# Performance work log

Measured on AMD Instinct MI355X. Metric: run time of the kernel, lower is better.

## Reference

```python
import jax, jax.numpy as jnp
import numpy as np

B, L, D, H, BS, R, MLP = 2, 4096, 768, 12, 64, 3, 3072
HD = D // H            # 64 head dim
NB = L // BS           # 64 blocks
EPS = 1e-6
SEED = 0               # connectivity_seed


def _rand_plan():
    """Static BigBird key-block plan for middle query blocks: [NB-2, 5+R].
    Columns: global first, global last, window (i-1, i, i+1), R random blocks."""
    rng = np.random.RandomState(SEED)
    rows = []
    for i in range(1, NB - 1):
        excl = {0, NB - 1, i - 1, i, i + 1}
        cand = np.array([j for j in range(NB) if j not in excl])
        rnd = rng.choice(cand, size=R, replace=False)
        rows.append(np.concatenate([np.array([0, NB - 1, i - 1, i, i + 1]), rnd]))
    return jnp.asarray(np.stack(rows), dtype=jnp.int32)

_PLAN = _rand_plan()


def _layernorm(x, scale, bias):
    mu = jnp.mean(x, axis=-1, keepdims=True)
    var = jnp.mean(jnp.square(x - mu), axis=-1, keepdims=True)
    return (x - mu) * jax.lax.rsqrt(var + EPS) * scale + bias


def _bigbird_attention(x, Wq, Wk, Wv, Wo):
    # projections: [B,L,D] x [D,H,HD] -> [B,H,L,HD]; flax scales q by 1/sqrt(HD)
    q = jnp.einsum('bld,dhk->bhlk', x, Wq) / jnp.sqrt(jnp.asarray(HD, x.dtype))
    k = jnp.einsum('bld,dhk->bhlk', x, Wk)
    v = jnp.einsum('bld,dhk->bhlk', x, Wv)
    qb = q.reshape(B, H, NB, BS, HD)
    kb = k.reshape(B, H, NB, BS, HD)
    vb = v.reshape(B, H, NB, BS, HD)
    # global query rows (first & last block) attend densely to all keys
    qg = qb[:, :, jnp.array([0, NB - 1])]                 # [B,H,2,BS,HD]
    sg = jnp.einsum('bhgqd,bhld->bhgql', qg, k)           # [B,H,2,BS,L]
    og = jnp.einsum('bhgql,bhld->bhgqd', jax.nn.softmax(sg, axis=-1), v)
    # middle query rows: gather window + global + random key blocks
    S = _PLAN.shape[1]                                     # 5 + R = 8 blocks
    km = kb[:, :, _PLAN].reshape(B, H, NB - 2, S * BS, HD)
    vm = vb[:, :, _PLAN].reshape(B, H, NB - 2, S * BS, HD)
    sm = jnp.einsum('bhmqd,bhmkd->bhmqk', qb[:, :, 1:NB - 1], km)
    om = jnp.einsum('bhmqk,bhmkd->bhmqd', jax.nn.softmax(sm, axis=-1), vm)
    ob = jnp.concatenate([og[:, :, :1], om, og[:, :, 1:]], axis=2)  # [B,H,NB,BS,HD]
    o = ob.reshape(B, H, L, HD)
    return jnp.einsum('bhlk,hkd->bld', o, Wo)


def setup_inputs() -> dict:
    key = jax.random.key(0)
    ks = jax.random.split(key, 8)
    s_qkv = (2.0 / (D + HD)) ** 0.5   # xavier-uniform-ish std
    s_mlp1 = (2.0 / (D + MLP)) ** 0.5
    return {
        'x': jax.random.normal(ks[0], (B, L, D), jnp.float32),
        'ln1_scale': jnp.ones((D,), jnp.float32),
        'ln1_bias': jnp.zeros((D,), jnp.float32),
        'Wq': jax.random.normal(ks[1], (D, H, HD), jnp.float32) * s_qkv,
        'Wk': jax.random.normal(ks[2], (D, H, HD), jnp.float32) * s_qkv,
        'Wv': jax.random.normal(ks[3], (D, H, HD), jnp.float32) * s_qkv,
        'Wo': jax.random.normal(ks[4], (H, HD, D), jnp.float32) * s_qkv,
        'ln2_scale': jnp.ones((D,), jnp.float32),
        'ln2_bias': jnp.zeros((D,), jnp.float32),
        'W1': jax.random.normal(ks[5], (D, MLP), jnp.float32) * s_mlp1,
        'b1': jnp.zeros((MLP,), jnp.float32),
        'W2': jax.random.normal(ks[6], (MLP, D), jnp.float32) * s_mlp1,
        'b2': jnp.zeros((D,), jnp.float32),
    }


def reference(x, ln1_scale, ln1_bias, Wq, Wk, Wv, Wo, ln2_scale, ln2_bias, W1, b1, W2, b2):
    h = _layernorm(x, ln1_scale, ln1_bias)
    attn = _bigbird_attention(h, Wq, Wk, Wv, Wo)
    x1 = attn + x                                  # residual (dropout deterministic)
    y = _layernorm(x1, ln2_scale, ln2_bias)
    y = jax.nn.relu(jnp.einsum('bld,df->blf', y, W1) + b1)
    y = jnp.einsum('blf,fd->bld', y, W2) + b2
    return x1 + y
```

## Files before the change

### kernel.cpp

```cpp
#include <hip/hip_runtime.h>
#include <stdint.h>

constexpr int D_MODEL = 768;
constexpr int SEQ     = 4096;
constexpr int NHEAD   = 12;
constexpr int HDIM    = 64;
constexpr int BATCH   = 2;
constexpr int DFF     = 3072;
constexpr int ROWS    = BATCH * SEQ;

typedef __attribute__((ext_vector_type(8))) __bf16 bfrag;
typedef __attribute__((ext_vector_type(8))) short  s16x8;
typedef __attribute__((ext_vector_type(4))) short  s16x4;
typedef __attribute__((ext_vector_type(4))) float  f32x4;

#define MFMA16(a, b, c) __builtin_amdgcn_mfma_f32_16x16x32_bf16((a), (b), (c), 0, 0, 0)
#define AS1(p) ((__attribute__((address_space(1))) void*)(uintptr_t)(p))
#define AS3(p) ((__attribute__((address_space(3))) void*)(p))

__device__ __forceinline__ float b2f(short s) {
  union { unsigned u; float f; } c;
  c.u = ((unsigned)(unsigned short)s) << 16;
  return c.f;
}
__device__ __forceinline__ short f2b(float f) {
  union { float f; unsigned u; } c;
  c.f = f;
  unsigned r = c.u + 0x7fffu + ((c.u >> 16) & 1u);
  return (short)(r >> 16);
}

struct PlanT { int v[64][8]; };

struct MTRng {
  unsigned mt[624];
  int mti;
  constexpr MTRng() : mt{}, mti(624) {
    mt[0] = 0u;
    for (int i = 1; i < 624; ++i)
      mt[i] = 1812433253u * (mt[i-1] ^ (mt[i-1] >> 30)) + (unsigned)i;
  }
  constexpr unsigned next() {
    if (mti >= 624) {
      for (int i = 0; i < 624; ++i) {
        unsigned y = (mt[i] & 0x80000000u) | (mt[(i+1) % 624] & 0x7fffffffu);
        unsigned v = mt[(i+397) % 624] ^ (y >> 1);
        if (y & 1u) v ^= 0x9908b0dfu;
        mt[i] = v;
      }
      mti = 0;
    }
    unsigned y = mt[mti++];
    y ^= y >> 11;
    y ^= (y << 7)  & 0x9d2c5680u;
    y ^= (y << 15) & 0xefc60000u;
    y ^= y >> 18;
    return y;
  }
  constexpr unsigned interval(unsigned mx) {
    unsigned mask = mx;
    mask |= mask >> 1; mask |= mask >> 2; mask |= mask >> 4;
    mask |= mask >> 8; mask |= mask >> 16;
    unsigned v = next() & mask;
    while (v > mx) v = next() & mask;
    return v;
  }
};

constexpr PlanT make_plan() {
  PlanT P{};
  MTRng rng{};
  for (int i = 1; i <= 62; ++i) {
    int cand[64] = {}; int n = 0;
    for (int j = 0; j < 64; ++j) {
      if (j == 0 || j == 63 || j == i-1 || j == i || j == i+1) continue;
      cand[n++] = j;
    }
    int perm[64] = {};
    for (int p = 0; p < n; ++p) perm[p] = p;
    for (int p = n - 1; p > 0; --p) {
      int j = (int)rng.interval((unsigned)p);
      int t = perm[p]; perm[p] = perm[j]; perm[j] = t;
    }
    P.v[i][0] = 0;  P.v[i][1] = 63; P.v[i][2] = i-1; P.v[i][3] = i; P.v[i][4] = i+1;
    P.v[i][5] = cand[perm[0]]; P.v[i][6] = cand[perm[1]]; P.v[i][7] = cand[perm[2]];
  }
  return P;
}
constexpr PlanT h_plan = make_plan();
__constant__ PlanT g_plan = h_plan;

__global__ __launch_bounds__(256) void ln_kernel(
    const float* __restrict__ x, const float* __restrict__ sc,
    const float* __restrict__ bi, short* __restrict__ y)
{
  const int row = blockIdx.x, tid = threadIdx.x;
  const size_t base = (size_t)row * D_MODEL;
  float v0 = x[base + tid], v1 = x[base + tid + 256], v2 = x[base + tid + 512];
  float s  = v0 + v1 + v2;
  float s2 = v0*v0 + v1*v1 + v2*v2;
  for (int off = 1; off < 64; off <<= 1) {
    s  += __shfl_xor(s,  off);
    s2 += __shfl_xor(s2, off);
  }
  __shared__ float red[8];
  if ((tid & 63) == 0) { red[tid >> 6] = s; red[4 + (tid >> 6)] = s2; }
  __syncthreads();
  s  = red[0] + red[1] + red[2] + red[3];
  s2 = red[4] + red[5] + red[6] + red[7];
  const float mu  = s * (1.f / 768.f);
  const float var = s2 * (1.f / 768.f) - mu * mu;
  const float rs  = rsqrtf(var + 1e-6f);
  short* yr = y + base;
  yr[tid]       = f2b((v0 - mu) * rs * sc[tid]       + bi[tid]);
  yr[tid + 256] = f2b((v1 - mu) * rs * sc[tid + 256] + bi[tid + 256]);
  yr[tid + 512] = f2b((v2 - mu) * rs * sc[tid + 512] + bi[tid + 512]);
}

struct TrArgs { const float* src[6]; short* dst[6]; };

__global__ __launch_bounds__(256) void tr_all(TrArgs a) {
  __shared__ short tile[32][33];
  const int idx = blockIdx.x;
  int w, bx, by, Rr, Cc;
  if (idx < 2304)      { w = idx / 576; int t = idx % 576;  bx = t % 24; by = t / 24; Rr = 768;  Cc = 768;  }
  else if (idx < 4608) { w = 4;         int t = idx - 2304; bx = t % 96; by = t / 96; Rr = 768;  Cc = 3072; }
  else                 { w = 5;         int t = idx - 4608; bx = t % 24; by = t / 24; Rr = 3072; Cc = 768;  }
  const float* in = a.src[w];
  short* out = a.dst[w];
  const int x0 = bx * 32, y0 = by * 32;
  const int tx = threadIdx.x & 31, ty = threadIdx.x >> 5;
  for (int i = 0; i < 32; i += 8)
    tile[ty + i][tx] = f2b(in[(size_t)(y0 + ty + i) * Cc + x0 + tx]);
  __syncthreads();
  for (int i = 0; i < 32; i += 8)
    out[(size_t)(x0 + ty + i) * Rr + y0 + tx] = tile[tx][ty + i];
}

enum { M_QKV = 0, M_RES = 3, M_BRELU = 4, M_BRES = 5 };

template <int MODE, int TN>
__global__ __launch_bounds__(256) void gemm_bt(
    const short* __restrict__ A, const short* __restrict__ Bt,
    void* __restrict__ Cv, short* __restrict__ C2, short* __restrict__ C3,
    const float* __restrict__ res, const float* __restrict__ bias, int N, int K)
{
  constexpr int NT = TN / 32;
  alignas(16) __shared__ short As[3][128 * 32];
  alignas(16) __shared__ short Bs[3][TN * 32];
  const int tid = threadIdx.x;
  const int wave = tid >> 6, lane = tid & 63;
  const int quad = lane >> 4, l15 = lane & 15;
  const int m0 = blockIdx.x * 128, n0 = blockIdx.y * TN;
  const int mw = (wave & 1) * 64, nw = (wave >> 1) * (TN / 2);

  f32x4 acc[4][NT];
#pragma unroll
  for (int i = 0; i < 4; ++i)
#pragma unroll
    for (int j = 0; j < NT; ++j) acc[i][j] = f32x4{0.f, 0.f, 0.f, 0.f};

  const int srow = wave * 32 + (lane >> 2);
  const int scol = (lane & 3) * 8;
  const size_t arow = (size_t)(m0 + srow) * K + scol;
  const size_t brow128 = (size_t)(n0 + srow) * K + scol;
  const size_t brow64  = (size_t)(n0 + wave * 16 + (lane >> 2)) * K + scol;

  auto STAGE = [&](int buf, int k0) {
    __builtin_amdgcn_global_load_lds(AS1(A + arow + k0),                AS3(As[buf] + (wave*32     ) * 32), 16, 0, 0);
    __builtin_amdgcn_global_load_lds(AS1(A + arow + k0 + (size_t)16*K), AS3(As[buf] + (wave*32 + 16) * 32), 16, 0, 0);
    if constexpr (TN == 128) {
      __builtin_amdgcn_global_load_lds(AS1(Bt + brow128 + k0),                AS3(Bs[buf] + (wave*32     ) * 32), 16, 0, 0);
      __builtin_amdgcn_global_load_lds(AS1(Bt + brow128 + k0 + (size_t)16*K), AS3(Bs[buf] + (wave*32 + 16) * 32), 16, 0, 0);
    } else {
      __builtin_amdgcn_global_load_lds(AS1(Bt + brow64 + k0), AS3(Bs[buf] + (wave*16) * 32), 16, 0, 0);
    }
  };

  STAGE(0, 0);

  int cb = 0;
  for (int k0 = 0; k0 < K; k0 += 32) {
    const int kn = k0 + 32;
    int sb = cb + 1; if (sb >= 3) sb -= 3;
    __builtin_amdgcn_sched_barrier(0);
    STAGE(sb, kn < K ? kn : 0);
    if constexpr (TN == 128) asm volatile("s_waitcnt vmcnt(4)" ::: "memory");
    else                     asm volatile("s_waitcnt vmcnt(3)" ::: "memory");
    __builtin_amdgcn_s_barrier();
    __builtin_amdgcn_sched_barrier(0);

    bfrag af[4], bfv[NT];
#pragma unroll
    for (int mt = 0; mt < 4; ++mt)  af[mt]  = *(const bfrag*)(As[cb] + (mw + mt*16 + l15) * 32 + quad * 8);
#pragma unroll
    for (int nt = 0; nt < NT; ++nt) bfv[nt] = *(const bfrag*)(Bs[cb] + (nw + nt*16 + l15) * 32 + quad * 8);
#pragma unroll
    for (int mt = 0; mt < 4; ++mt)
#pragma unroll
      for (int nt = 0; nt < NT; ++nt)
        acc[mt][nt] = MFMA16(af[mt], bfv[nt], acc[mt][nt]);

    cb = sb;
  }
  asm volatile("s_waitcnt vmcnt(0)" ::: "memory");

#pragma unroll
  for (int mt = 0; mt < 4; ++mt) {
#pragma unroll
    for (int nt = 0; nt < NT; ++nt) {
      if (MODE == M_QKV) {
        const int gn = n0 + nw + nt*16 + l15;
        const int seg = gn / 768, gn2 = gn - seg * 768;
        const int gm0 = m0 + mw + mt*16 + quad*4;
        if (seg == 2) {
          const int bb = gm0 >> 12, l = gm0 & 4095, hh = gn2 >> 6, hd = gn2 & 63;
          s16x4 pk{f2b(acc[mt][nt][0]), f2b(acc[mt][nt][1]),
                   f2b(acc[mt][nt][2]), f2b(acc[mt][nt][3])};
          *(s16x4*)(&C3[(((size_t)(bb * NHEAD + hh)) * HDIM + hd) * SEQ + l]) = pk;
        } else {
#pragma unroll
          for (int r = 0; r < 4; ++r) {
            const float v = acc[mt][nt][r];
            if (seg == 0) ((short*)Cv)[(size_t)(gm0 + r) * 768 + gn2] = f2b(v * 0.125f);
            else          C2[(size_t)(gm0 + r) * 768 + gn2] = f2b(v);
          }
        }
      } else {
#pragma unroll
        for (int r = 0; r < 4; ++r) {
          const int gm = m0 + mw + mt*16 + quad*4 + r;
          const int gn = n0 + nw + nt*16 + l15;
          float v = acc[mt][nt][r];
          const size_t ci = (size_t)gm * N + gn;
          if (MODE == M_RES)   { ((float*)Cv)[ci] = v + res[ci]; }
          if (MODE == M_BRELU) { v += bias[gn]; ((short*)Cv)[ci] = f2b(v > 0.f ? v : 0.f); }
          if (MODE == M_BRES)  { ((float*)Cv)[ci] = v + bias[gn] + res[ci]; }
        }
      }
    }
  }
}

constexpr int PSTR = 72;
constexpr int KSTR = 68;

__global__ __launch_bounds__(256, 3) void attn_kernel(
    const short* __restrict__ q, const short* __restrict__ k,
    const short* __restrict__ vt, short* __restrict__ o,
    short* __restrict__ Opart, float* __restrict__ ml)
{
  alignas(16) __shared__ short KV[4][64 * KSTR];
  alignas(16) __shared__ short Pbuf[4][2 * 16 * PSTR];
  const int xi = blockIdx.x, h = blockIdx.y, b = blockIdx.z;
  const int tid = threadIdx.x, wave = tid >> 6, lane = tid & 63;
  const int quad = lane >> 4, l15 = lane & 15;
  const int r8 = lane >> 3, g8 = lane & 7;

  int qb, part = 0, g = 0;
  bool partial;
  if (xi < 62) { qb = xi + 1; partial = false; }
  else { const int t = xi - 62; g = t >> 3; part = t & 7; qb = g ? 63 : 0; partial = true; }

  const short* qp = q + (size_t)(b * SEQ + qb * 64 + wave * 16 + l15) * D_MODEL + h * HDIM;
  const bfrag qf0 = *(const bfrag*)(qp + quad * 8);
  const bfrag qf1 = *(const bfrag*)(qp + 32 + quad * 8);

  const short* kb_base = k  + (size_t)b * SEQ * D_MODEL + h * HDIM;
  const short* vt_base = vt + ((size_t)(b * NHEAD + h)) * HDIM * SEQ;

  const int sr0 = wave * 16 + r8, sr1 = wave * 16 + 8 + r8;

  auto kidx = [&](int t, int which) -> int {
    const int tt = t > 3 ? 3 : t;
    return partial ? (part * 8 + 2 * tt + which) : g_plan.v[qb][2 * tt + which];
  };
  auto load8 = [&](int k0i, int k1i, s16x8* R) {
    const short* ka = kb_base + (size_t)k0i * 64 * D_MODEL + g8 * 8;
    const short* kbp = kb_base + (size_t)k1i * 64 * D_MODEL + g8 * 8;
    const short* va = vt_base + (size_t)k0i * 64 + g8 * 8;
    const short* vb = vt_base + (size_t)k1i * 64 + g8 * 8;
    R[0] = *(const s16x8*)(ka  + (size_t)sr0 * D_MODEL);
    R[1] = *(const s16x8*)(ka  + (size_t)sr1 * D_MODEL);
    R[2] = *(const s16x8*)(kbp + (size_t)sr0 * D_MODEL);
    R[3] = *(const s16x8*)(kbp + (size_t)sr1 * D_MODEL);
    R[4] = *(const s16x8*)(va  + (size_t)sr0 * SEQ);
    R[5] = *(const s16x8*)(va  + (size_t)sr1 * SEQ);
    R[6] = *(const s16x8*)(vb  + (size_t)sr0 * SEQ);
    R[7] = *(const s16x8*)(vb  + (size_t)sr1 * SEQ);
  };

  float m_r[4], l_r[4];
  f32x4 oacc[4];
#pragma unroll
  for (int r = 0; r < 4; ++r) { m_r[r] = -1e9f; l_r[r] = 0.f; }
#pragma unroll
  for (int nt = 0; nt < 4; ++nt) oacc[nt] = f32x4{0.f, 0.f, 0.f, 0.f};

  short* pb = &Pbuf[wave][0];

  s16x8 R[8];
  load8(kidx(0, 0), kidx(0, 1), R);

  for (int it = 0; it < 4; ++it) {
    __syncthreads();
#pragma unroll
    for (int bu = 0; bu < 4; ++bu) {
      *(s16x8*)(&KV[bu][sr0 * KSTR + g8 * 8]) = R[2 * bu];
      *(s16x8*)(&KV[bu][sr1 * KSTR + g8 * 8]) = R[2 * bu + 1];
    }
    __syncthreads();

    load8(kidx(it + 1, 0), kidx(it + 1, 1), R);

    f32x4 s0[4], s1[4];
#pragma unroll
    for (int nt = 0; nt < 4; ++nt) {
      const int fr = (nt * 16 + l15) * KSTR + quad * 8;
      const bfrag ka0 = *(const bfrag*)(&KV[0][fr]);
      const bfrag ka1 = *(const bfrag*)(&KV[0][fr + 32]);
      const bfrag kb0 = *(const bfrag*)(&KV[1][fr]);
      const bfrag kb1 = *(const bfrag*)(&KV[1][fr + 32]);
      s0[nt] = f32x4{0.f,0.f,0.f,0.f}; s1[nt] = f32x4{0.f,0.f,0.f,0.f};
      s0[nt] = MFMA16(qf0, ka0, s0[nt]); s0[nt] = MFMA16(qf1, ka1, s0[nt]);
      s1[nt] = MFMA16(qf0, kb0, s1[nt]); s1[nt] = MFMA16(qf1, kb1, s1[nt]);
    }

    float alpha[4];
#pragma unroll
    for (int r = 0; r < 4; ++r) {
      float v = fmaxf(fmaxf(fmaxf(s0[0][r], s0[1][r]), fmaxf(s0[2][r], s0[3][r])),
                      fmaxf(fmaxf(s1[0][r], s1[1][r]), fmaxf(s1[2][r], s1[3][r])));
      v = fmaxf(v, __shfl_xor(v, 1));
      v = fmaxf(v, __shfl_xor(v, 2));
      v = fmaxf(v, __shfl_xor(v, 4));
      v = fmaxf(v, __shfl_xor(v, 8));
      const float mn = fmaxf(m_r[r], v);
      alpha[r] = __expf(m_r[r] - mn);
      m_r[r] = mn;
    }
    float psum[4] = {0.f, 0.f, 0.f, 0.f};
#pragma unroll
    for (int nt = 0; nt < 4; ++nt)
#pragma unroll
      for (int r = 0; r < 4; ++r) {
        const float p0 = __expf(s0[nt][r] - m_r[r]);
        const float p1 = __expf(s1[nt][r] - m_r[r]);
        s0[nt][r] = p0; s1[nt][r] = p1;
        psum[r] += p0 + p1;
      }
#pragma unroll
    for (int r = 0; r < 4; ++r) {
      float v = psum[r];
      v += __shfl_xor(v, 1); v += __shfl_xor(v, 2);
      v += __shfl_xor(v, 4); v += __shfl_xor(v, 8);
      l_r[r] = l_r[r] * alpha[r] + v;
    }

#pragma unroll
    for (int nt = 0; nt < 4; ++nt)
#pragma unroll
      for (int r = 0; r < 4; ++r) {
        pb[(quad * 4 + r) * PSTR + nt * 16 + l15]             = f2b(s0[nt][r]);
        pb[16 * PSTR + (quad * 4 + r) * PSTR + nt * 16 + l15] = f2b(s1[nt][r]);
      }

#pragma unroll
    for (int nt = 0; nt < 4; ++nt)
#pragma unroll
      for (int r = 0; r < 4; ++r) oacc[nt][r] *= alpha[r];
#pragma unroll
    for (int s = 0; s < 2; ++s) {
      const bfrag pf0 = *(const bfrag*)(pb + l15 * PSTR + s * 32 + quad * 8);
      const bfrag pf1 = *(const bfrag*)(pb + 16 * PSTR + l15 * PSTR + s * 32 + quad * 8);
#pragma unroll
      for (int nt = 0; nt < 4; ++nt) {
        const int fr = (nt * 16 + l15) * KSTR + s * 32 + quad * 8;
        const bfrag vf0 = *(const bfrag*)(&KV[2][fr]);
        const bfrag vf1 = *(const bfrag*)(&KV[3][fr]);
        oacc[nt] = MFMA16(pf0, vf0, oacc[nt]);
        oacc[nt] = MFMA16(pf1, vf1, oacc[nt]);
      }
    }
  }

  if (!partial) {
    short* op = o + (size_t)(b * SEQ + qb * 64 + wave * 16) * D_MODEL + h * HDIM;
#pragma unroll
    for (int r = 0; r < 4; ++r) {
      const float inv = 1.f / l_r[r];
#pragma unroll
      for (int nt = 0; nt < 4; ++nt)
        op[(size_t)(quad * 4 + r) * D_MODEL + nt * 16 + l15] = f2b(oacc[nt][r] * inv);
    }
  } else {
    const int pi = ((b * NHEAD + h) * 2 + g) * 8 + part;
    short* Op = Opart + (size_t)pi * 4096;
    float* mp = ml + (size_t)pi * 128;
#pragma unroll
    for (int r = 0; r < 4; ++r) {
      const int row = wave * 16 + quad * 4 + r;
#pragma unroll
      for (int nt = 0; nt < 4; ++nt)
        Op[row * 64 + nt * 16 + l15] = f2b(oacc[nt][r]);
      if (l15 == 0) { mp[row] = m_r[r]; mp[64 + row] = l_r[r]; }
    }
  }
}

__global__ __launch_bounds__(256) void attn_merge(
    const short* __restrict__ Opart, const float* __restrict__ ml,
    short* __restrict__ o)
{
  const int bi = blockIdx.x;
  const int g = bi & 1, h = (bi >> 1) % NHEAD, b = bi / (2 * NHEAD);
  const int qb = g ? 63 : 0;
  const int pi0 = bi * 8;
#pragma unroll
  for (int e = 0; e < 16; ++e) {
    const int idx = threadIdx.x + e * 256;
    const int r = idx >> 6, c = idx & 63;
    float ms = -1e9f;
#pragma unroll
    for (int p = 0; p < 8; ++p) ms = fmaxf(ms, ml[(size_t)(pi0 + p) * 128 + r]);
    float lsum = 0.f, osum = 0.f;
#pragma unroll
    for (int p = 0; p < 8; ++p) {
      const float w = __expf(ml[(size_t)(pi0 + p) * 128 + r] - ms);
      lsum += w * ml[(size_t)(pi0 + p) * 128 + 64 + r];
      osum += w * b2f(Opart[(size_t)(pi0 + p) * 4096 + idx]);
    }
    o[(size_t)(b * SEQ + qb * 64 + r) * D_MODEL + h * HDIM + c] = f2b(osum / lsum);
  }
}

extern "C" void kernel_launch(void* const* d_in, const int* in_sizes, int n_in,
                              void* d_out, int out_size, void* d_ws, size_t ws_size,
                              hipStream_t stream) {
  (void)in_sizes; (void)n_in; (void)out_size; (void)ws_size;
  const float* x    = (const float*)d_in[0];
  const float* ln1s = (const float*)d_in[1];
  const float* ln1b = (const float*)d_in[2];
  const float* Wq   = (const float*)d_in[3];
  const float* Wk   = (const float*)d_in[4];
  const float* Wv   = (const float*)d_in[5];
  const float* Wo   = (const float*)d_in[6];
  const float* ln2s = (const float*)d_in[7];
  const float* ln2b = (const float*)d_in[8];
  const float* W1   = (const float*)d_in[9];
  const float* b1   = (const float*)d_in[10];
  const float* W2   = (const float*)d_in[11];
  const float* b2   = (const float*)d_in[12];
  float* out = (float*)d_out;

  short* WqT  = (short*)((char*)d_ws + 256);
  short* WkT  = WqT  + 768 * 768;
  short* WvT  = WkT  + 768 * 768;
  short* WoT  = WvT  + 768 * 768;
  short* W1T  = WoT  + 768 * 768;
  short* W2T  = W1T  + (size_t)3072 * 768;
  short* hbuf = W2T  + (size_t)3072 * 768;
  short* qbuf = hbuf + (size_t)ROWS * D_MODEL;
  short* kbuf = qbuf + (size_t)ROWS * D_MODEL;
  short* vtb  = kbuf + (size_t)ROWS * D_MODEL;
  short* obuf = vtb  + (size_t)ROWS * D_MODEL;
  short* tbuf = qbuf;
  short* Opart = hbuf;
  float* mlbuf = (float*)(hbuf + (size_t)384 * 4096);

  TrArgs ta;
  ta.src[0] = Wq; ta.src[1] = Wk; ta.src[2] = Wv; ta.src[3] = Wo; ta.src[4] = W1; ta.src[5] = W2;
  ta.dst[0] = WqT; ta.dst[1] = WkT; ta.dst[2] = WvT; ta.dst[3] = WoT; ta.dst[4] = W1T; ta.dst[5] = W2T;
  tr_all<<<6912, 256, 0, stream>>>(ta);

  ln_kernel<<<ROWS, 256, 0, stream>>>(x, ln1s, ln1b, hbuf);

  gemm_bt<M_QKV, 128><<<dim3(64, 18), 256, 0, stream>>>(hbuf, WqT, qbuf, kbuf, vtb, nullptr, nullptr, 2304, 768);

  attn_kernel<<<dim3(78, 12, 2), 256, 0, stream>>>(qbuf, kbuf, vtb, obuf, Opart, mlbuf);
  attn_merge<<<48, 256, 0, stream>>>(Opart, mlbuf, obuf);

  gemm_bt<M_RES, 64><<<dim3(64, 12), 256, 0, stream>>>(obuf, WoT, out, nullptr, nullptr, x, nullptr, 768, 768);

  ln_kernel<<<ROWS, 256, 0, stream>>>(out, ln2s, ln2b, hbuf);

  gemm_bt<M_BRELU, 128><<<dim3(64, 24), 256, 0, stream>>>(hbuf, W1T, tbuf, nullptr, nullptr, nullptr, b1, 3072, 768);
  gemm_bt<M_BRES, 64> <<<dim3(64, 12), 256, 0, stream>>>(tbuf, W2T, out, nullptr, nullptr, out, b2, 768, 3072);
}
```

Before: 354.3 us.

## Split-K the W2 GEMM with atomic adds and load attention K/V directly

The final MLP down-projection now splits K into two halves over a z grid dimension. Each half atomically adds its partial sum plus half the bias into the output, which already holds the residual, so the grid gets twice the blocks for the long-K GEMM. Separately, the attention kernel drops its LDS staging of K/V tiles and the associated barriers, reading MFMA fragments straight from global memory. This trades explicit prefetch and shared reuse for fewer syncs and less LDS. The atomics make the summation order nondeterministic and add atomic traffic.

```diff
diff --git a/kernel.cpp b/kernel.cpp
--- a/kernel.cpp
+++ b/kernel.cpp
@@ -28,6 +28,15 @@
   c.f = f;
   unsigned r = c.u + 0x7fffu + ((c.u >> 16) & 1u);
   return (short)(r >> 16);
+}
+
+__device__ __forceinline__ void atomAddF(float* p, float v) {
+#if __has_builtin(__builtin_amdgcn_global_atomic_fadd_f32)
+  (void)__builtin_amdgcn_global_atomic_fadd_f32(
+      (__attribute__((address_space(1))) float*)(uintptr_t)p, v);
+#else
+  atomicAdd(p, v);
+#endif
 }
 
 struct PlanT { int v[64][8]; };
@@ -137,13 +146,14 @@
     out[(size_t)(x0 + ty + i) * Rr + y0 + tx] = tile[tx][ty + i];
 }
 
-enum { M_QKV = 0, M_RES = 3, M_BRELU = 4, M_BRES = 5 };
+enum { M_QKV = 0, M_RES = 3, M_BRELU = 4, M_BRES_AT = 6 };
 
 template <int MODE, int TN>
 __global__ __launch_bounds__(256) void gemm_bt(
     const short* __restrict__ A, const short* __restrict__ Bt,
     void* __restrict__ Cv, short* __restrict__ C2, short* __restrict__ C3,
-    const float* __restrict__ res, const float* __restrict__ bias, int N, int K)
+    const float* __restrict__ res, const float* __restrict__ bias,
+    int N, int K, int Ks)
 {
   constexpr int NT = TN / 32;
   alignas(16) __shared__ short As[3][128 * 32];
@@ -152,6 +162,7 @@
   const int wave = tid >> 6, lane = tid & 63;
   const int quad = lane >> 4, l15 = lane & 15;
   const int m0 = blockIdx.x * 128, n0 = blockIdx.y * TN;
+  const int kbeg = blockIdx.z * Ks, kend = kbeg + Ks;
   const int mw = (wave & 1) * 64, nw = (wave >> 1) * (TN / 2);
 
   f32x4 acc[4][NT];
@@ -177,14 +188,14 @@
     }
   };
 
-  STAGE(0, 0);
+  STAGE(0, kbeg);
 
   int cb = 0;
-  for (int k0 = 0; k0 < K; k0 += 32) {
+  for (int k0 = kbeg; k0 < kend; k0 += 32) {
     const int kn = k0 + 32;
     int sb = cb + 1; if (sb >= 3) sb -= 3;
     __builtin_amdgcn_sched_barrier(0);
-    STAGE(sb, kn < K ? kn : 0);
+    STAGE(sb, kn < kend ? kn : kbeg);
     if constexpr (TN == 128) asm volatile("s_waitcnt vmcnt(4)" ::: "memory");
     else                     asm volatile("s_waitcnt vmcnt(3)" ::: "memory");
     __builtin_amdgcn_s_barrier();
@@ -233,9 +244,9 @@
           const int gn = n0 + nw + nt*16 + l15;
           float v = acc[mt][nt][r];
           const size_t ci = (size_t)gm * N + gn;
-          if (MODE == M_RES)   { ((float*)Cv)[ci] = v + res[ci]; }
-          if (MODE == M_BRELU) { v += bias[gn]; ((short*)Cv)[ci] = f2b(v > 0.f ? v : 0.f); }
-          if (MODE == M_BRES)  { ((float*)Cv)[ci] = v + bias[gn] + res[ci]; }
+          if (MODE == M_RES)     { ((float*)Cv)[ci] = v + res[ci]; }
+          if (MODE == M_BRELU)   { v += bias[gn]; ((short*)Cv)[ci] = f2b(v > 0.f ? v : 0.f); }
+          if (MODE == M_BRES_AT) { atomAddF((float*)Cv + ci, v + 0.5f * bias[gn]); }
         }
       }
     }
@@ -243,19 +254,16 @@
 }
 
 constexpr int PSTR = 72;
-constexpr int KSTR = 68;
 
 __global__ __launch_bounds__(256, 3) void attn_kernel(
     const short* __restrict__ q, const short* __restrict__ k,
     const short* __restrict__ vt, short* __restrict__ o,
     short* __restrict__ Opart, float* __restrict__ ml)
 {
-  alignas(16) __shared__ short KV[4][64 * KSTR];
   alignas(16) __shared__ short Pbuf[4][2 * 16 * PSTR];
   const int xi = blockIdx.x, h = blockIdx.y, b = blockIdx.z;
   const int tid = threadIdx.x, wave = tid >> 6, lane = tid & 63;
   const int quad = lane >> 4, l15 = lane & 15;
-  const int r8 = lane >> 3, g8 = lane & 7;
 
   int qb, part = 0, g = 0;
   bool partial;
@@ -269,25 +277,8 @@
   const short* kb_base = k  + (size_t)b * SEQ * D_MODEL + h * HDIM;
   const short* vt_base = vt + ((size_t)(b * NHEAD + h)) * HDIM * SEQ;
 
-  const int sr0 = wave * 16 + r8, sr1 = wave * 16 + 8 + r8;
-
   auto kidx = [&](int t, int which) -> int {
-    const int tt = t > 3 ? 3 : t;
-    return partial ? (part * 8 + 2 * tt + which) : g_plan.v[qb][2 * tt + which];
-  };
-  auto load8 = [&](int k0i, int k1i, s16x8* R) {
-    const short* ka = kb_base + (size_t)k0i * 64 * D_MODEL + g8 * 8;
-    const short* kbp = kb_base + (size_t)k1i * 64 * D_MODEL + g8 * 8;
-    const short* va = vt_base + (size_t)k0i * 64 + g8 * 8;
-    const short* vb = vt_base + (size_t)k1i * 64 + g8 * 8;
-    R[0] = *(const s16x8*)(ka  + (size_t)sr0 * D_MODEL);
-    R[1] = *(const s16x8*)(ka  + (size_t)sr1 * D_MODEL);
-    R[2] = *(const s16x8*)(kbp + (size_t)sr0 * D_MODEL);
-    R[3] = *(const s16x8*)(kbp + (size_t)sr1 * D_MODEL);
-    R[4] = *(const s16x8*)(va  + (size_t)sr0 * SEQ);
-    R[5] = *(const s16x8*)(va  + (size_t)sr1 * SEQ);
-    R[6] = *(const s16x8*)(vb  + (size_t)sr0 * SEQ);
-    R[7] = *(const s16x8*)(vb  + (size_t)sr1 * SEQ);
+    return partial ? (part * 8 + 2 * t + which) : g_plan.v[qb][2 * t + which];
   };
 
   float m_r[4], l_r[4];
@@ -299,28 +290,19 @@
 
   short* pb = &Pbuf[wave][0];
 
-  s16x8 R[8];
-  load8(kidx(0, 0), kidx(0, 1), R);
-
   for (int it = 0; it < 4; ++it) {
-    __syncthreads();
-#pragma unroll
-    for (int bu = 0; bu < 4; ++bu) {
-      *(s16x8*)(&KV[bu][sr0 * KSTR + g8 * 8]) = R[2 * bu];
-      *(s16x8*)(&KV[bu][sr1 * KSTR + g8 * 8]) = R[2 * bu + 1];
-    }
-    __syncthreads();
-
-    load8(kidx(it + 1, 0), kidx(it + 1, 1), R);
+    const int k0i = kidx(it, 0), k1i = kidx(it, 1);
+    const short* ka_t = kb_base + (size_t)k0i * 64 * D_MODEL;
+    const short* kb_t = kb_base + (size_t)k1i * 64 * D_MODEL;
 
     f32x4 s0[4], s1[4];
 #pragma unroll
     for (int nt = 0; nt < 4; ++nt) {
-      const int fr = (nt * 16 + l15) * KSTR + quad * 8;
-      const bfrag ka0 = *(const bfrag*)(&KV[0][fr]);
-      const bfrag ka1 = *(const bfrag*)(&KV[0][fr + 32]);
-      const bfrag kb0 = *(const bfrag*)(&KV[1][fr]);
-      const bfrag kb1 = *(const bfrag*)(&KV[1][fr + 32]);
+      const size_t krow = (size_t)(nt * 16 + l15) * D_MODEL + quad * 8;
+      const bfrag ka0 = *(const bfrag*)(ka_t + krow);
+      const bfrag ka1 = *(const bfrag*)(ka_t + krow + 32);
+      const bfrag kb0 = *(const bfrag*)(kb_t + krow);
+      const bfrag kb1 = *(const bfrag*)(kb_t + krow + 32);
       s0[nt] = f32x4{0.f,0.f,0.f,0.f}; s1[nt] = f32x4{0.f,0.f,0.f,0.f};
       s0[nt] = MFMA16(qf0, ka0, s0[nt]); s0[nt] = MFMA16(qf1, ka1, s0[nt]);
       s1[nt] = MFMA16(qf0, kb0, s1[nt]); s1[nt] = MFMA16(qf1, kb1, s1[nt]);
@@ -375,9 +357,9 @@
       const bfrag pf1 = *(const bfrag*)(pb + 16 * PSTR + l15 * PSTR + s * 32 + quad * 8);
 #pragma unroll
       for (int nt = 0; nt < 4; ++nt) {
-        const int fr = (nt * 16 + l15) * KSTR + s * 32 + quad * 8;
-        const bfrag vf0 = *(const bfrag*)(&KV[2][fr]);
-        const bfrag vf1 = *(const bfrag*)(&KV[3][fr]);
+        const size_t vrow = (size_t)(nt * 16 + l15) * SEQ + s * 32 + quad * 8;
+        const bfrag vf0 = *(const bfrag*)(vt_base + vrow + k0i * 64);
+        const bfrag vf1 = *(const bfrag*)(vt_base + vrow + k1i * 64);
         oacc[nt] = MFMA16(pf0, vf0, oacc[nt]);
         oacc[nt] = MFMA16(pf1, vf1, oacc[nt]);
       }
@@ -475,15 +457,15 @@
 
   ln_kernel<<<ROWS, 256, 0, stream>>>(x, ln1s, ln1b, hbuf);
 
-  gemm_bt<M_QKV, 128><<<dim3(64, 18), 256, 0, stream>>>(hbuf, WqT, qbuf, kbuf, vtb, nullptr, nullptr, 2304, 768);
+  gemm_bt<M_QKV, 128><<<dim3(64, 18), 256, 0, stream>>>(hbuf, WqT, qbuf, kbuf, vtb, nullptr, nullptr, 2304, 768, 768);
 
   attn_kernel<<<dim3(78, 12, 2), 256, 0, stream>>>(qbuf, kbuf, vtb, obuf, Opart, mlbuf);
   attn_merge<<<48, 256, 0, stream>>>(Opart, mlbuf, obuf);
 
-  gemm_bt<M_RES, 64><<<dim3(64, 12), 256, 0, stream>>>(obuf, WoT, out, nullptr, nullptr, x, nullptr, 768, 768);
+  gemm_bt<M_RES, 64><<<dim3(64, 12), 256, 0, stream>>>(obuf, WoT, out, nullptr, nullptr, x, nullptr, 768, 768, 768);
 
   ln_kernel<<<ROWS, 256, 0, stream>>>(out, ln2s, ln2b, hbuf);
 
-  gemm_bt<M_BRELU, 128><<<dim3(64, 24), 256, 0, stream>>>(hbuf, W1T, tbuf, nullptr, nullptr, nullptr, b1, 3072, 768);
-  gemm_bt<M_BRES, 64> <<<dim3(64, 12), 256, 0, stream>>>(tbuf, W2T, out, nullptr, nullptr, out, b2, 768, 3072);
-}
+  gemm_bt<M_BRELU, 128><<<dim3(64, 24), 256, 0, stream>>>(hbuf, W1T, tbuf, nullptr, nullptr, nullptr, b1, 3072, 768, 768);
+  gemm_bt<M_BRES_AT, 64><<<dim3(64, 12, 2), 256, 0, stream>>>(tbuf, W2T, out, nullptr, nullptr, nullptr, b2, 768, 3072, 1536);
+}
```

Result: slower. 453.4 us (+28.0%).
